# Optimization experiments

Measured on AMD Instinct MI355X. Metric: run time of the kernel, lower is better.

The kernel has to match this reference:

```python
import math
import jax, jax.numpy as jnp
import numpy as np

N_HEAD = 16
KNN = 4                     # config.knn_num
MEM_FRAC = 8.0              # config.mem_frac
INFLUENCE = 1.0             # config.knn_softmax_influence
RESID_FOUND = 0.5           # from set_resid_frac(resid_frac=0.5) (assumed split)
RESID_CURR = 0.5


def setup_inputs() -> dict:
    key = jax.random.key(0)
    ks = jax.random.split(key, 7)
    B, T, C, H, M = 1, 1024, 1024, N_HEAD, 8192
    d = C // H
    return {
        "x": jax.random.normal(ks[0], (B, T, C), jnp.float32),
        "c_attn_w": jax.random.normal(ks[1], (3 * C, C), jnp.float32) * 0.02,
        "c_attn_b": jax.random.normal(ks[2], (3 * C,), jnp.float32) * 0.01,
        "c_proj_w": jax.random.normal(ks[3], (C, C), jnp.float32) * 0.02,
        "c_proj_b": jax.random.normal(ks[4], (C,), jnp.float32) * 0.01,
        "key_store": jax.random.normal(ks[5], (H, M, d), jnp.float32),
        "value_store": jax.random.normal(ks[6], (H, M, d), jnp.float32),
    }


def _knn_get(att, k, q, v, key_store, value_store):
    # Faithful vectorized version of knn_get (batch must be 1, as in the
    # original whose scatter offsets i*t are only valid for b==1).
    B, H, T, d = k.shape
    scale = 1.0 / math.sqrt(d)
    # last-query attention row over all keys: (B,H,T)
    a = att[:, :, -1, :]
    # mem_frac thresholding (bookkeeping_frac falsy -> skipped)
    a = jnp.where(a < 1.0 / (MEM_FRAC * T), 0.0, a)
    sel = (a != 0.0)[0]                      # (H,T) selected positions
    kh, qh, vh = k[0], q[0], v[0]            # (H,T,d)
    # exact L2 search = faiss.IndexFlatL2: d2 = |k|^2 - 2 k.s + |s|^2
    d2 = (jnp.sum(kh * kh, -1, keepdims=True)
          - 2.0 * jnp.einsum('htd,hmd->htm', kh, key_store)
          + jnp.sum(key_store * key_store, -1)[:, None, :])   # (H,T,M)
    _, idx = jax.lax.top_k(-d2, KNN)         # (H,T,K) nearest neighbors
    idx = jnp.maximum(idx, 0)                # idx[idx<0]=0
    keys_f = jnp.take_along_axis(key_store[:, None, :, :], idx[..., None], axis=2)   # (H,T,K,d)
    vals_f = jnp.take_along_axis(value_store[:, None, :, :], idx[..., None], axis=2)
    # not resid_only: prepend current key/value -> stack size K+1
    keys_all = jnp.concatenate([kh[:, :, None, :], keys_f], axis=2)   # (H,T,S,d)
    vals_all = jnp.concatenate([vh[:, :, None, :], vals_f], axis=2)
    attf = jnp.einsum('htd,htsd->hts', qh, keys_all) * scale
    attf = jnp.where(jnp.isnan(attf), -jnp.inf, attf)
    w = jax.nn.softmax(attf * INFLUENCE, axis=-1)                     # softmax over the stack dim
    vals = jnp.einsum('hts,htsd->htd', w, vals_all)
    vals = vals * RESID_FOUND + vh * RESID_CURR                       # resid mix branch
    v_new = jnp.where(sel[..., None], vals, vh)                       # scatter back
    return v_new[None]                                                # (1,H,T,d)


def reference(x, c_attn_w, c_attn_b, c_proj_w, c_proj_b, key_store, value_store):
    B, T, C = x.shape
    H = key_store.shape[0]
    d = C // H
    qkv = x @ c_attn_w.T + c_attn_b
    q, k, v = jnp.split(qkv, 3, axis=2)
    heads = lambda t: t.reshape(B, T, H, d).transpose(0, 2, 1, 3)
    q, k, v = heads(q), heads(k), heads(v)
    logits = jnp.einsum('bhqd,bhkd->bhqk', q, k) * (1.0 / math.sqrt(d))
    causal = jnp.tril(jnp.ones((T, T), bool))
    logits = jnp.where(causal, logits, -jnp.inf)
    att = jax.nn.softmax(logits, axis=-1)
    # knn_get runs under torch.no_grad in the original
    v_new = jax.lax.stop_gradient(_knn_get(att, k, q, v, key_store, value_store))
    y = jnp.einsum('bhqk,bhkd->bhqd', att, v_new)   # dropout p=0 (eval)
    y = y.transpose(0, 2, 1, 3).reshape(B, T, C)
    return y @ c_proj_w.T + c_proj_b
```

## Files before the change

kernel.cpp:

```cpp
#include <hip/hip_runtime.h>
#include <math.h>

#define NH 16
#define TT 1024
#define CC 1024
#define DD 64
#define MM 8192
#define MQ 4
#define MQS (MM / MQ)

typedef __attribute__((ext_vector_type(8))) short short8;
typedef __attribute__((ext_vector_type(4))) float f32x4;

__device__ __forceinline__ float wredsum(float x) {
#pragma unroll
  for (int o = 32; o; o >>= 1) x += __shfl_xor(x, o);
  return x;
}
__device__ __forceinline__ unsigned int bf16rn(float x) {
  unsigned int u = __float_as_uint(x);
  return (u + 0x7fffu + ((u >> 16) & 1u)) >> 16;
}
__device__ __forceinline__ float bf16f(unsigned int h) {
  return __uint_as_float(h << 16);
}

__device__ __forceinline__ void ins4(float d, int i, float vd[4], int vi[4]) {
  if (d < vd[3] || (d == vd[3] && i < vi[3])) {
    vd[3] = d; vi[3] = i;
#pragma unroll
    for (int s = 3; s > 0; --s) {
      bool sw = (vd[s] < vd[s - 1]) || (vd[s] == vd[s - 1] && vi[s] < vi[s - 1]);
      if (sw) {
        float td = vd[s]; vd[s] = vd[s - 1]; vd[s - 1] = td;
        int ti = vi[s]; vi[s] = vi[s - 1]; vi[s - 1] = ti;
      }
    }
  }
}

__device__ __forceinline__ void stage_rows8_swz(const char* gRow0, size_t gStride, char* lds, int lane) {
  int rr = lane >> 3;
  int c = (lane & 7) ^ rr;
  __builtin_amdgcn_global_load_lds(
      (const __attribute__((address_space(1))) unsigned int*)(gRow0 + (size_t)rr * gStride + (c << 4)),
      (__attribute__((address_space(3))) unsigned int*)lds, 16, 0, 0);
}

__device__ __forceinline__ void conv_chunk(const float* __restrict__ src,
                                           char* __restrict__ hi, char* __restrict__ lo, int gc) {
  const float* p = src + ((size_t)gc << 3);
  float4 f0 = *(const float4*)p;
  float4 f1 = *(const float4*)(p + 4);
  float f[8] = {f0.x, f0.y, f0.z, f0.w, f1.x, f1.y, f1.z, f1.w};
  short8 hv, lv;
#pragma unroll
  for (int e = 0; e < 8; ++e) {
    unsigned hb = bf16rn(f[e]);
    hv[e] = (short)hb;
    lv[e] = (short)bf16rn(f[e] - bf16f(hb));
  }
  size_t off = (size_t)gc << 4;
  *(short8*)(hi + off) = hv;
  *(short8*)(lo + off) = lv;
}

__global__ void __launch_bounds__(256) convert_all(
    const float* __restrict__ x, char* __restrict__ xhi, char* __restrict__ xlo,
    const float* __restrict__ Wa, char* __restrict__ wahi, char* __restrict__ walo,
    const float* __restrict__ Wp, char* __restrict__ wphi, char* __restrict__ wplo)
{
  int b = blockIdx.x, tid = threadIdx.x;
  if (b < 512) conv_chunk(x, xhi, xlo, b * 256 + tid);
  else if (b < 2048) conv_chunk(Wa, wahi, walo, (b - 512) * 256 + tid);
  else conv_chunk(Wp, wphi, wplo, (b - 2048) * 256 + tid);
}

__global__ void __launch_bounds__(256) convert_kernel(
    const float* __restrict__ ks, char* __restrict__ khi,
    char* __restrict__ klo, float* __restrict__ kn2)
{
  int gc = blockIdx.x * 256 + threadIdx.x;
  const float* p = ks + ((size_t)gc << 3);
  float4 f0 = *(const float4*)p;
  float4 f1 = *(const float4*)(p + 4);
  float f[8] = {f0.x, f0.y, f0.z, f0.w, f1.x, f1.y, f1.z, f1.w};
  float s = 0.f;
  short8 hv, lv;
#pragma unroll
  for (int e = 0; e < 8; ++e) {
    s = fmaf(f[e], f[e], s);
    unsigned hb = bf16rn(f[e]);
    hv[e] = (short)hb;
    lv[e] = (short)bf16rn(f[e] - bf16f(hb));
  }
  size_t off = (size_t)gc << 4;
  *(short8*)(khi + off) = hv;
  *(short8*)(klo + off) = lv;
  s += __shfl_xor(s, 1);
  s += __shfl_xor(s, 2);
  s += __shfl_xor(s, 4);
  if ((threadIdx.x & 7) == 0) kn2[gc >> 3] = -0.5f * s;
}

__global__ void __launch_bounds__(256) gemm_hl(
    const char* __restrict__ Ahi, const char* __restrict__ Alo, int strideA, int aKb0, int aKbz,
    const char* __restrict__ Bhi, const char* __restrict__ Blo, int strideB, int bKb0, int bKbz,
    int kbBeg, int kbCnt, int kbzStep,
    float* __restrict__ Cf, long long czMul, int ldc,
    const float* __restrict__ bias, float scale)
{
  int bx = blockIdx.x, by = blockIdx.y, z = blockIdx.z;
  int n0 = bx * 128, m0 = by * 128;
  int tid = threadIdx.x, lane = tid & 63, w = tid >> 6;
  int wr = w >> 1, wc = w & 1;
  __shared__ __align__(16) char smem[65536];
  char* sAhi = smem;
  char* sAlo = smem + 16384;
  char* sBhi = smem + 32768;
  char* sBlo = smem + 49152;
  f32x4 acc[4][4];
#pragma unroll
  for (int i = 0; i < 4; ++i)
#pragma unroll
    for (int j = 0; j < 4; ++j) acc[i][j] = (f32x4){0.f, 0.f, 0.f, 0.f};

  int kb0 = kbBeg + z * kbzStep;
  int lr = lane & 15, lc = lane >> 4;
  for (int i = 0; i < kbCnt; ++i) {
    int kbA = aKb0 + z * aKbz + kb0 + i;
    int kbB = bKb0 + z * bKbz + kb0 + i;
    if (i) __syncthreads();
#pragma unroll
    for (int c8 = 0; c8 < 4; ++c8) {
      int r8 = w * 32 + c8 * 8;
      stage_rows8_swz(Ahi + (size_t)(m0 + r8) * strideA + (size_t)kbA * 128, strideA, sAhi + r8 * 128, lane);
      stage_rows8_swz(Alo + (size_t)(m0 + r8) * strideA + (size_t)kbA * 128, strideA, sAlo + r8 * 128, lane);
      stage_rows8_swz(Bhi + (size_t)(n0 + r8) * strideB + (size_t)kbB * 128, strideB, sBhi + r8 * 128, lane);
      stage_rows8_swz(Blo + (size_t)(n0 + r8) * strideB + (size_t)kbB * 128, strideB, sBlo + r8 * 128, lane);
    }
    __syncthreads();
#pragma unroll
    for (int kh = 0; kh < 2; ++kh) {
      short8 ah[4], al[4], bh[4], bl[4];
#pragma unroll
      for (int f = 0; f < 4; ++f) {
        int ra = wr * 64 + f * 16 + lr;
        int ca = ((kh * 4 + lc) ^ (ra & 7)) << 4;
        ah[f] = *(const short8*)(sAhi + ra * 128 + ca);
        al[f] = *(const short8*)(sAlo + ra * 128 + ca);
        int rb = wc * 64 + f * 16 + lr;
        int cb = ((kh * 4 + lc) ^ (rb & 7)) << 4;
        bh[f] = *(const short8*)(sBhi + rb * 128 + cb);
        bl[f] = *(const short8*)(sBlo + rb * 128 + cb);
      }
#pragma unroll
      for (int mi = 0; mi < 4; ++mi)
#pragma unroll
        for (int nj = 0; nj < 4; ++nj) {
          acc[mi][nj] = __builtin_amdgcn_mfma_f32_16x16x32_bf16(ah[mi], bh[nj], acc[mi][nj], 0, 0, 0);
          acc[mi][nj] = __builtin_amdgcn_mfma_f32_16x16x32_bf16(al[mi], bh[nj], acc[mi][nj], 0, 0, 0);
          acc[mi][nj] = __builtin_amdgcn_mfma_f32_16x16x32_bf16(ah[mi], bl[nj], acc[mi][nj], 0, 0, 0);
        }
    }
  }
#pragma unroll
  for (int mi = 0; mi < 4; ++mi)
#pragma unroll
    for (int nj = 0; nj < 4; ++nj)
#pragma unroll
      for (int r = 0; r < 4; ++r) {
        int m = m0 + wr * 64 + mi * 16 + lc * 4 + r;
        int n = n0 + wc * 64 + nj * 16 + lr;
        float v = acc[mi][nj][r] * scale;
        if (bias) v += bias[n];
        Cf[(size_t)z * czMul + (size_t)m * ldc + n] = v;
      }
}

__global__ void __launch_bounds__(256) reduce_qkv(
    const float* __restrict__ p, const float* __restrict__ bias,
    char* __restrict__ hi, char* __restrict__ lo)
{
  int gc = blockIdx.x * 256 + threadIdx.x;
  int t = gc / 384, c = gc - t * 384;
  const float* p0 = p + (size_t)t * 3072 + (c << 3);
  const float* p1 = p0 + (size_t)3072 * 1024;
  float4 a0 = *(const float4*)p0, a1 = *(const float4*)(p0 + 4);
  float4 b0 = *(const float4*)p1, b1 = *(const float4*)(p1 + 4);
  float4 bb0 = *(const float4*)(bias + (c << 3));
  float4 bb1 = *(const float4*)(bias + (c << 3) + 4);
  float f[8] = {a0.x + b0.x + bb0.x, a0.y + b0.y + bb0.y,
                a0.z + b0.z + bb0.z, a0.w + b0.w + bb0.w,
                a1.x + b1.x + bb1.x, a1.y + b1.y + bb1.y,
                a1.z + b1.z + bb1.z, a1.w + b1.w + bb1.w};
  short8 hv, lv;
#pragma unroll
  for (int e = 0; e < 8; ++e) {
    unsigned hb = bf16rn(f[e]);
    hv[e] = (short)hb;
    lv[e] = (short)bf16rn(f[e] - bf16f(hb));
  }
  size_t off = (size_t)gc << 4;
  *(short8*)(hi + off) = hv;
  *(short8*)(lo + off) = lv;
}

#define QSLDS 2304
__global__ void __launch_bounds__(512) qk_softmax(
    const char* __restrict__ qhi, const char* __restrict__ qlo,
    char* __restrict__ attB, float* __restrict__ attlast)
{
  int rb = blockIdx.x, h = blockIdx.y;
  int i0 = rb * 32;
  int tid = threadIdx.x, lane = tid & 63, w = tid >> 6;
  int wr = w >> 2, wcg = w & 3;
  int lr = lane & 15, lc = lane >> 4;
  __shared__ float redm[2][16][4];
  __shared__ float reds[2][16][4];
  __shared__ __align__(16) char tb[8][2 * QSLDS];

  int iq = i0 + wr * 16 + lr;
  short8 ah[2], al[2];
  {
    size_t qb = (size_t)iq * 6144 + h * 128;
#pragma unroll
    for (int kh = 0; kh < 2; ++kh) {
      size_t off = qb + ((kh * 4 + lc) << 4);
      ah[kh] = *(const short8*)(qhi + off);
      al[kh] = *(const short8*)(qlo + off);
    }
  }

  f32x4 acc[16];
#pragma unroll
  for (int nt = 0; nt < 16; ++nt) acc[nt] = (f32x4){0.f, 0.f, 0.f, 0.f};

  int maxj = i0 + 31;
#pragma unroll
  for (int nt = 0; nt < 16; ++nt) {
    if (wcg * 256 + nt * 16 <= maxj) {
      int jr = wcg * 256 + nt * 16 + lr;
      size_t kb = (size_t)jr * 6144 + 2048 + h * 128;
      short8 bh[2], bl[2];
#pragma unroll
      for (int kh = 0; kh < 2; ++kh) {
        size_t off = kb + ((kh * 4 + lc) << 4);
        bh[kh] = *(const short8*)(qhi + off);
        bl[kh] = *(const short8*)(qlo + off);
      }
#pragma unroll
      for (int kh = 0; kh < 2; ++kh) {
        acc[nt] = __builtin_amdgcn_mfma_f32_16x16x32_bf16(ah[kh], bh[kh], acc[nt], 0, 0, 0);
        acc[nt] = __builtin_amdgcn_mfma_f32_16x16x32_bf16(al[kh], bh[kh], acc[nt], 0, 0, 0);
        acc[nt] = __builtin_amdgcn_mfma_f32_16x16x32_bf16(ah[kh], bl[kh], acc[nt], 0, 0, 0);
      }
    }
  }

  int iv[4];
  float pmax[4];
#pragma unroll
  for (int r = 0; r < 4; ++r) {
    iv[r] = i0 + wr * 16 + lc * 4 + r;
    pmax[r] = -INFINITY;
  }
#pragma unroll
  for (int nt = 0; nt < 16; ++nt) {
    int j = wcg * 256 + nt * 16 + lr;
#pragma unroll
    for (int r = 0; r < 4; ++r) {
      float v = (j <= iv[r]) ? acc[nt][r] * 0.125f : -INFINITY;
      acc[nt][r] = v;
      pmax[r] = fmaxf(pmax[r], v);
    }
  }
#pragma unroll
  for (int o = 1; o <= 8; o <<= 1)
#pragma unroll
    for (int r = 0; r < 4; ++r) pmax[r] = fmaxf(pmax[r], __shfl_xor(pmax[r], o));
  if (lr == 0) {
#pragma unroll
    for (int r = 0; r < 4; ++r) redm[wr][lc * 4 + r][wcg] = pmax[r];
  }
  __syncthreads();
  float rowm[4];
#pragma unroll
  for (int r = 0; r < 4; ++r) {
    float* q = redm[wr][lc * 4 + r];
    rowm[r] = fmaxf(fmaxf(q[0], q[1]), fmaxf(q[2], q[3]));
  }

  float psum[4] = {0.f, 0.f, 0.f, 0.f};
#pragma unroll
  for (int nt = 0; nt < 16; ++nt)
#pragma unroll
    for (int r = 0; r < 4; ++r) {
      float e = __expf(acc[nt][r] - rowm[r]);
      acc[nt][r] = e;
      psum[r] += e;
    }
#pragma unroll
  for (int o = 1; o <= 8; o <<= 1)
#pragma unroll
    for (int r = 0; r < 4; ++r) psum[r] += __shfl_xor(psum[r], o);
  if (lr == 0) {
#pragma unroll
    for (int r = 0; r < 4; ++r) reds[wr][lc * 4 + r][wcg] = psum[r];
  }
  __syncthreads();
  float inv[4];
#pragma unroll
  for (int r = 0; r < 4; ++r) {
    float* q = reds[wr][lc * 4 + r];
    inv[r] = 1.0f / (q[0] + q[1] + q[2] + q[3]);
  }

  char* mybuf = tb[w];
  int iv0 = i0 + wr * 16;
#pragma unroll
  for (int cc = 0; cc < 4; ++cc) {
#pragma unroll
    for (int q = 0; q < 4; ++q) {
      int nt = cc * 4 + q;
      int col = q * 16 + lr;
#pragma unroll
      for (int r = 0; r < 4; ++r) {
        int row = lc * 4 + r;
        float v = acc[nt][r] * inv[r];
        unsigned hb = bf16rn(v);
        unsigned lb = bf16rn(v - bf16f(hb));
        *(unsigned short*)(mybuf + row * 144 + col * 2) = (unsigned short)hb;
        *(unsigned short*)(mybuf + QSLDS + row * 144 + col * 2) = (unsigned short)lb;
        if (iv[r] == 1023) attlast[(h << 10) + wcg * 256 + cc * 64 + col] = v;
      }
    }
    __syncthreads();
#pragma unroll
    for (int half = 0; half < 2; ++half) {
      int rr = (lane >> 3) + half * 8;
      int c = lane & 7;
      int rowg = iv0 + rr;
      uint4 hv = *(const uint4*)(mybuf + rr * 144 + c * 16);
      uint4 lv = *(const uint4*)(mybuf + QSLDS + rr * 144 + c * 16);
      size_t basep = ((size_t)h << 22) + ((size_t)rowg << 12)
                   + (size_t)(((wcg << 2) + cc) << 7) + (size_t)(c << 4);
      *(uint4*)(attB + basep) = hv;
      *(uint4*)(attB + basep + 2048) = lv;
    }
    __syncthreads();
  }
}

#define BUFB 16384

#define TOPK_STEP(PAR, DO_STAGE)                                              \
  {                                                                           \
    if (DO_STAGE) {                                                           \
      _Pragma("unroll")                                                       \
      for (int i2 = 0; i2 < 4; ++i2) {                                        \
        __builtin_amdgcn_global_load_lds(                                     \
            (const __attribute__((address_space(1))) unsigned int*)stsrc[i2], \
            (__attribute__((address_space(3))) unsigned int*)(stdst[i2] + ((PAR) ^ 16384)), \
            16, 0, 0);                                                        \
        stsrc[i2] += 8192;                                                    \
      }                                                                       \
    }                                                                         \
    f32x4 acc[4];                                                             \
    _Pragma("unroll")                                                         \
    for (int ms = 0; ms < 4; ++ms)                                            \
      acc[ms] = *(const f32x4*)(knp + ms * 64);                               \
    knp += 256;                                                               \
    _Pragma("unroll")                                                         \
    for (int ms = 0; ms < 4; ++ms) {                                          \
      short8 ah0 = *(const short8*)(frg[ms * 2 + 0] + (PAR));                 \
      short8 al0 = *(const short8*)(frg[ms * 2 + 0] + (PAR) + 8192);          \
      short8 ah1 = *(const short8*)(frg[ms * 2 + 1] + (PAR));                 \
      short8 al1 = *(const short8*)(frg[ms * 2 + 1] + (PAR) + 8192);          \
      acc[ms] = __builtin_amdgcn_mfma_f32_16x16x32_bf16(ah0, bhi[0], acc[ms], 0, 0, 0); \
      acc[ms] = __builtin_amdgcn_mfma_f32_16x16x32_bf16(al0, bhi[0], acc[ms], 0, 0, 0); \
      acc[ms] = __builtin_amdgcn_mfma_f32_16x16x32_bf16(ah0, blo[0], acc[ms], 0, 0, 0); \
      acc[ms] = __builtin_amdgcn_mfma_f32_16x16x32_bf16(ah1, bhi[1], acc[ms], 0, 0, 0); \
      acc[ms] = __builtin_amdgcn_mfma_f32_16x16x32_bf16(al1, bhi[1], acc[ms], 0, 0, 0); \
      acc[ms] = __builtin_amdgcn_mfma_f32_16x16x32_bf16(ah1, blo[1], acc[ms], 0, 0, 0); \
    }                                                                         \
    float pk[16];                                                             \
    _Pragma("unroll")                                                         \
    for (int ms = 0; ms < 4; ++ms)                                            \
      _Pragma("unroll")                                                       \
      for (int r = 0; r < 4; ++r) {                                           \
        unsigned u = __float_as_uint(acc[ms][r]);                             \
        pk[ms * 4 + r] = __uint_as_float((u & ~15u) | (unsigned)(ms * 4 + r)); \
      }                                                                       \
    float mx = pk[0];                                                         \
    _Pragma("unroll")                                                         \
    for (int c = 1; c < 16; ++c) mx = fmaxf(mx, pk[c]);                       \
    while (mx > ba[3]) {                                                      \
      unsigned pb = __float_as_uint(mx);                                      \
      int cl = pb & 15;                                                       \
      ba[3] = mx; bi_[3] = mg0 + ((cl & 12) << 2) + (cl & 3);                 \
      _Pragma("unroll")                                                       \
      for (int s = 3; s > 0; --s)                                             \
        if (ba[s] > ba[s - 1]) {                                              \
          float td = ba[s]; ba[s] = ba[s - 1]; ba[s - 1] = td;                \
          int ti = bi_[s]; bi_[s] = bi_[s - 1]; bi_[s - 1] = ti;              \
        }                                                                     \
      _Pragma("unroll")                                                       \
      for (int c2 = 0; c2 < 16; ++c2)                                         \
        if (pk[c2] == mx) pk[c2] = -3.0e38f;                                  \
      mx = pk[0];                                                             \
      _Pragma("unroll")                                                       \
      for (int c2 = 1; c2 < 16; ++c2) mx = fmaxf(mx, pk[c2]);                 \
    }                                                                         \
    mg0 += 64;                                                                \
    __syncthreads();                                                          \
  }

__global__ void __launch_bounds__(256, 4) topk_mfma(
    const char* __restrict__ qhi, const char* __restrict__ qlo,
    const char* __restrict__ khi, const char* __restrict__ klo,
    const float* __restrict__ kn2, float* __restrict__ pd, int* __restrict__ pi)
{
  int bid = blockIdx.x;
  int h = bid & 15, ttile = (bid >> 4) & 15, mq = bid >> 8;
  int tid = threadIdx.x, lane = tid & 63, w = tid >> 6;
  int t0 = ttile * 64 + w * 16;
  __shared__ __align__(16) char smem[2 * BUFB];

  short8 bhi[2], blo[2];
  {
    int t = t0 + (lane & 15);
    size_t rb = (size_t)t * 6144 + 2048 + h * 128;
#pragma unroll
    for (int kh = 0; kh < 2; ++kh) {
      size_t off = rb + ((kh * 4 + (lane >> 4)) << 4);
      bhi[kh] = *(const short8*)(qhi + off);
      blo[kh] = *(const short8*)(qlo + off);
    }
  }

  const char* ghi = khi + ((size_t)h * MM + (size_t)mq * MQS) * 128;
  const char* glo = klo + ((size_t)h * MM + (size_t)mq * MQS) * 128;
  const char* knp = (const char*)(kn2 + (size_t)h * MM + (size_t)mq * MQS + ((lane >> 4) << 2));

  float ba[4] = {-3.0e38f, -3.0e38f, -3.0e38f, -3.0e38f};
  int   bi_[4] = {-1, -1, -1, -1};

  const char* stsrc[4];
  char* stdst[4];
  {
    int rr = lane >> 3;
    size_t laneoff = (size_t)rr * 128 + (((lane & 7) ^ rr) << 4);
#pragma unroll
    for (int i2 = 0; i2 < 4; ++i2) {
      int s = w * 4 + i2;
      stsrc[i2] = ((s < 8) ? (ghi + s * 1024) : (glo + (s - 8) * 1024)) + laneoff;
      stdst[i2] = smem + s * 1024;
    }
  }
  char* frg[8];
#pragma unroll
  for (int ms = 0; ms < 4; ++ms)
#pragma unroll
    for (int kh = 0; kh < 2; ++kh) {
      int mloc = ms * 16 + (lane & 15);
      int c = kh * 4 + (lane >> 4);
      frg[ms * 2 + kh] = smem + mloc * 128 + ((c ^ (mloc & 7)) << 4);
    }

#pragma unroll
  for (int i2 = 0; i2 < 4; ++i2) {
    __builtin_amdgcn_global_load_lds(
        (const __attribute__((address_space(1))) unsigned int*)stsrc[i2],
        (__attribute__((address_space(3))) unsigned int*)stdst[i2], 16, 0, 0);
    stsrc[i2] += 8192;
  }
  __syncthreads();

  int mg0 = mq * MQS + ((lane >> 4) << 2);
  for (int it2 = 0; it2 < 16; ++it2) {
    TOPK_STEP(0, true)
    TOPK_STEP(16384, (it2 < 15))
  }

  float bd[4];
#pragma unroll
  for (int s = 0; s < 4; ++s) bd[s] = ba[s] * -2.0f;
#pragma unroll
  for (int st = 16; st <= 32; st <<= 1) {
    float sd[4]; int si[4];
#pragma unroll
    for (int s = 0; s < 4; ++s) {
      sd[s] = __shfl_xor(bd[s], st);
      si[s] = __shfl_xor(bi_[s], st);
    }
#pragma unroll
    for (int s = 0; s < 4; ++s) ins4(sd[s], si[s], bd, bi_);
  }
  if (lane < 16) {
    size_t o = (((size_t)mq * NH + h) * TT + (t0 + lane)) * 4;
#pragma unroll
    for (int s = 0; s < 4; ++s) { pd[o + s] = bd[s]; pi[o + s] = bi_[s]; }
  }
}

__global__ void __launch_bounds__(1024) knn_attend(
    const char* __restrict__ qhi, const char* __restrict__ qlo,
    const float* __restrict__ attlast,
    const float* __restrict__ pd, const int* __restrict__ pi,
    const float* __restrict__ kstore, const float* __restrict__ vstore,
    char* __restrict__ vThi, char* __restrict__ vTlo)
{
  __shared__ __align__(16) unsigned short hiT[64][72];
  __shared__ __align__(16) unsigned short loT[64][72];
  int tid = threadIdx.x, lane = tid & 63, w = tid >> 6;
  int h = blockIdx.x >> 4, t0 = (blockIdx.x & 15) << 6;

#pragma unroll
  for (int i = 0; i < 4; ++i) {
    int t = t0 + w * 4 + i;
    int g = (h << 10) + t;

    float fd[4]; int fi[4];
    {
      size_t o = ((size_t)(lane & 3) * (NH * TT) + g) * 4;
#pragma unroll
      for (int s = 0; s < 4; ++s) { fd[s] = pd[o + s]; fi[s] = pi[o + s]; }
#pragma unroll
      for (int st = 1; st <= 2; st <<= 1) {
        float sd[4]; int si[4];
#pragma unroll
        for (int s = 0; s < 4; ++s) {
          sd[s] = __shfl_xor(fd[s], st);
          si[s] = __shfl_xor(fi[s], st);
        }
#pragma unroll
        for (int s = 0; s < 4; ++s) ins4(sd[s], si[s], fd, fi);
      }
    }

    size_t rb = (size_t)t * 6144 + h * 128 + lane * 2;
    float q = bf16f(*(const unsigned short*)(qhi + rb)) + bf16f(*(const unsigned short*)(qlo + rb));
    float k = bf16f(*(const unsigned short*)(qhi + rb + 2048)) + bf16f(*(const unsigned short*)(qlo + rb + 2048));
    float v = bf16f(*(const unsigned short*)(qhi + rb + 4096)) + bf16f(*(const unsigned short*)(qlo + rb + 4096));
    float al = attlast[g];
    bool sel = al >= (1.0f / 8192.0f);

    float attf[5], vf[5];
    attf[0] = wredsum(q * k) * 0.125f;
    vf[0] = v;
#pragma unroll
    for (int s = 1; s < 5; ++s) {
      int m = fi[s - 1];
      const float* kp = kstore + ((size_t)h * MM + m) * DD;
      const float* vp = vstore + ((size_t)h * MM + m) * DD;
      attf[s] = wredsum(q * kp[lane]) * 0.125f;
      vf[s] = vp[lane];
    }
    float mx = attf[0];
#pragma unroll
    for (int s = 1; s < 5; ++s) mx = fmaxf(mx, attf[s]);
    float wgt[5], sum = 0.f;
#pragma unroll
    for (int s = 0; s < 5; ++s) { wgt[s] = __expf(attf[s] - mx); sum += wgt[s]; }
    float inv = 1.0f / sum;
    float vals = 0.f;
#pragma unroll
    for (int s = 0; s < 5; ++s) vals = fmaf(wgt[s] * inv, vf[s], vals);
    float r = 0.5f * vals + 0.5f * v;
    float vn = sel ? r : v;

    unsigned hb = bf16rn(vn);
    hiT[lane][t - t0] = (unsigned short)hb;
    loT[lane][t - t0] = (unsigned short)bf16rn(vn - bf16f(hb));
  }
  __syncthreads();

  int half = tid >> 9;
  int idx = tid & 511;
  int r = idx >> 3, c = idx & 7;
  const unsigned short* src = half ? &loT[r][c * 8] : &hiT[r][c * 8];
  uint4 vv = *(const uint4*)src;
  char* dst = (half ? vTlo : vThi) + (size_t)((h << 6) + r) * 2048 + ((size_t)t0 << 1) + (c << 4);
  *(uint4*)dst = vv;
}

__global__ void __launch_bounds__(256) gemm_attv(
    const char* __restrict__ attB, const char* __restrict__ vThi, const char* __restrict__ vTlo,
    char* __restrict__ Yhi, char* __restrict__ Ylo)
{
  int h = blockIdx.y, m0 = blockIdx.x * 128;
  const char* aBase = attB + (size_t)h * 4194304;
  int tid = threadIdx.x, lane = tid & 63, w = tid >> 6;
  int wr = w >> 1, wc = w & 1;
  __shared__ __align__(16) char smem[49152];
  char* sAhi = smem;
  char* sAlo = smem + 16384;
  char* sBhi = smem + 32768;
  char* sBlo = smem + 40960;
  f32x4 acc[4][2];
#pragma unroll
  for (int i = 0; i < 4; ++i)
#pragma unroll
    for (int j = 0; j < 2; ++j) acc[i][j] = (f32x4){0.f, 0.f, 0.f, 0.f};
  int lr = lane & 15, lc = lane >> 4;
  int kbEnd = ((m0 + 127) >> 6) + 1;
  if (kbEnd > 16) kbEnd = 16;
  for (int kb = 0; kb < kbEnd; ++kb) {
    if (kb) __syncthreads();
#pragma unroll
    for (int c8 = 0; c8 < 4; ++c8) {
      int r8 = w * 32 + c8 * 8;
      stage_rows8_swz(aBase + (size_t)(m0 + r8) * 4096 + (size_t)kb * 128, 4096, sAhi + r8 * 128, lane);
      stage_rows8_swz(aBase + (size_t)(m0 + r8) * 4096 + 2048 + (size_t)kb * 128, 4096, sAlo + r8 * 128, lane);
    }
#pragma unroll
    for (int c8 = 0; c8 < 2; ++c8) {
      int r8 = w * 16 + c8 * 8;
      stage_rows8_swz(vThi + (size_t)((h << 6) + r8) * 2048 + (size_t)kb * 128, 2048, sBhi + r8 * 128, lane);
      stage_rows8_swz(vTlo + (size_t)((h << 6) + r8) * 2048 + (size_t)kb * 128, 2048, sBlo + r8 * 128, lane);
    }
    __syncthreads();
#pragma unroll
    for (int kh = 0; kh < 2; ++kh) {
      short8 ah[4], al[4], bh[2], bl[2];
#pragma unroll
      for (int f = 0; f < 4; ++f) {
        int ra = wr * 64 + f * 16 + lr;
        int ca = ((kh * 4 + lc) ^ (ra & 7)) << 4;
        ah[f] = *(const short8*)(sAhi + ra * 128 + ca);
        al[f] = *(const short8*)(sAlo + ra * 128 + ca);
      }
#pragma unroll
      for (int f = 0; f < 2; ++f) {
        int rbr = wc * 32 + f * 16 + lr;
        int cb = ((kh * 4 + lc) ^ (rbr & 7)) << 4;
        bh[f] = *(const short8*)(sBhi + rbr * 128 + cb);
        bl[f] = *(const short8*)(sBlo + rbr * 128 + cb);
      }
#pragma unroll
      for (int mi = 0; mi < 4; ++mi)
#pragma unroll
        for (int nj = 0; nj < 2; ++nj) {
          acc[mi][nj] = __builtin_amdgcn_mfma_f32_16x16x32_bf16(ah[mi], bh[nj], acc[mi][nj], 0, 0, 0);
          acc[mi][nj] = __builtin_amdgcn_mfma_f32_16x16x32_bf16(al[mi], bh[nj], acc[mi][nj], 0, 0, 0);
          acc[mi][nj] = __builtin_amdgcn_mfma_f32_16x16x32_bf16(ah[mi], bl[nj], acc[mi][nj], 0, 0, 0);
        }
    }
  }
#pragma unroll
  for (int mi = 0; mi < 4; ++mi)
#pragma unroll
    for (int nj = 0; nj < 2; ++nj)
#pragma unroll
      for (int r = 0; r < 4; ++r) {
        int m = m0 + wr * 64 + mi * 16 + lc * 4 + r;
        int n = (h << 6) + wc * 32 + nj * 16 + lr;
        float v = acc[mi][nj][r];
        unsigned hb = bf16rn(v);
        size_t off = ((size_t)m * 1024 + n) * 2;
        *(unsigned short*)(Yhi + off) = (unsigned short)hb;
        *(unsigned short*)(Ylo + off) = (unsigned short)bf16rn(v - bf16f(hb));
      }
}

__global__ void __launch_bounds__(256) reduce_bias(
    const float* __restrict__ p, const float* __restrict__ bias, float* __restrict__ out)
{
  int i4 = blockIdx.x * 256 + threadIdx.x;
  const float4* P = (const float4*)p;
  float4 a = P[i4], b = P[i4 + 262144], c = P[i4 + 524288], d = P[i4 + 786432];
  float4 bb = ((const float4*)bias)[i4 & 255];
  float4 o;
  o.x = a.x + b.x + c.x + d.x + bb.x;
  o.y = a.y + b.y + c.y + d.y + bb.y;
  o.z = a.z + b.z + c.z + d.z + bb.z;
  o.w = a.w + b.w + c.w + d.w + bb.w;
  ((float4*)out)[i4] = o;
}

extern "C" void kernel_launch(void* const* d_in, const int* in_sizes, int n_in,
                              void* d_out, int out_size, void* d_ws, size_t ws_size,
                              hipStream_t stream) {
  (void)in_sizes; (void)n_in; (void)out_size; (void)ws_size;
  const float* x  = (const float*)d_in[0];
  const float* Wa = (const float*)d_in[1];
  const float* ba = (const float*)d_in[2];
  const float* Wp = (const float*)d_in[3];
  const float* bp = (const float*)d_in[4];
  const float* Ks = (const float*)d_in[5];
  const float* Vs = (const float*)d_in[6];
  float* out = (float*)d_out;

  char* base = (char*)d_ws;
  char* xhi  = base;
  char* xlo  = base + 0x200000;
  char* wahi = base + 0x400000;
  char* walo = base + 0xA00000;
  char* khi  = base + 0x1000000;
  char* klo  = base + 0x2000000;
  float* qkvp = (float*)(base + 0x1000000);
  char*  attB = base;
  float* pout = (float*)base;
  char* tail = base + 0x4000000;
  char* qhi = tail;
  char* qlo = tail + 0x600000;
  float* attlast = (float*)(tail + 0xC00000);
  float* kn2     = (float*)(tail + 0xC10000);
  float* pd      = (float*)(tail + 0xC90000);
  int*   pi      = (int*)(tail + 0xE90000);
  char* vThi = tail + 0x1090000;
  char* vTlo = tail + 0x1290000;
  char* yhi  = tail + 0x1490000;
  char* ylo  = tail + 0x1690000;
  char* wphi = tail + 0x1890000;
  char* wplo = tail + 0x1A90000;

  hipLaunchKernelGGL(convert_all, dim3(2560), dim3(256), 0, stream,
                     x, xhi, xlo, Wa, wahi, walo, Wp, wphi, wplo);
  hipLaunchKernelGGL(gemm_hl, dim3(24, 8, 2), dim3(256), 0, stream,
                     (const char*)xhi, (const char*)xlo, 2048, 0, 0,
                     (const char*)wahi, (const char*)walo, 2048, 0, 0,
                     0, 8, 8,
                     qkvp, 3145728LL, 3072,
                     (const float*)nullptr, 1.0f);
  hipLaunchKernelGGL(reduce_qkv, dim3(1536), dim3(256), 0, stream, qkvp, ba, qhi, qlo);
  hipLaunchKernelGGL(convert_kernel, dim3(NH * MM * 8 / 256), dim3(256), 0, stream, Ks, khi, klo, kn2);
  hipLaunchKernelGGL(topk_mfma, dim3(16 * 16 * MQ), dim3(256), 0, stream,
                     (const char*)qhi, (const char*)qlo, (const char*)khi, (const char*)klo,
                     kn2, pd, pi);
  hipLaunchKernelGGL(qk_softmax, dim3(32, 16), dim3(512), 0, stream,
                     (const char*)qhi, (const char*)qlo, attB, attlast);
  hipLaunchKernelGGL(knn_attend, dim3(256), dim3(1024), 0, stream,
                     (const char*)qhi, (const char*)qlo, attlast, pd, pi, Ks, Vs, vThi, vTlo);
  hipLaunchKernelGGL(gemm_attv, dim3(8, 16), dim3(256), 0, stream,
                     (const char*)attB, (const char*)vThi, (const char*)vTlo, yhi, ylo);
  hipLaunchKernelGGL(gemm_hl, dim3(8, 8, 4), dim3(256), 0, stream,
                     (const char*)yhi, (const char*)ylo, 2048, 0, 0,
                     (const char*)wphi, (const char*)wplo, 2048, 0, 0,
                     0, 4, 4,
                     pout, 1048576LL, 1024,
                     (const float*)nullptr, 1.0f);
  hipLaunchKernelGGL(reduce_bias, dim3(1024), dim3(256), 0, stream, pout, bp, out);
}
```

Baseline: 225.9 us.

## Replace split-K GEMMs and reduce kernels with fused-epilogue GEMMs, merge convert kernels

Drops the split-K QKV and output projection GEMMs and their separate reduce kernels. In their place come dedicated GEMMs with smaller tiles: 64x128 for QKV, with bias add and hi/lo bf16 split done in the epilogue through LDS, and 64x64 for the output projection, with bias written straight to the output. The key-store conversion is also folded into the convert_all launch. The aim is to cut launches and the float partial-sum round trips through global memory. The cost is less parallelism per tile and the full K loop running in each block.

```diff
diff --git a/kernel.cpp b/kernel.cpp
--- a/kernel.cpp
+++ b/kernel.cpp
@@ -68,19 +68,15 @@
 __global__ void __launch_bounds__(256) convert_all(
     const float* __restrict__ x, char* __restrict__ xhi, char* __restrict__ xlo,
     const float* __restrict__ Wa, char* __restrict__ wahi, char* __restrict__ walo,
-    const float* __restrict__ Wp, char* __restrict__ wphi, char* __restrict__ wplo)
+    const float* __restrict__ Wp, char* __restrict__ wphi, char* __restrict__ wplo,
+    const float* __restrict__ ks, char* __restrict__ khi, char* __restrict__ klo,
+    float* __restrict__ kn2)
 {
   int b = blockIdx.x, tid = threadIdx.x;
-  if (b < 512) conv_chunk(x, xhi, xlo, b * 256 + tid);
-  else if (b < 2048) conv_chunk(Wa, wahi, walo, (b - 512) * 256 + tid);
-  else conv_chunk(Wp, wphi, wplo, (b - 2048) * 256 + tid);
-}
-
-__global__ void __launch_bounds__(256) convert_kernel(
-    const float* __restrict__ ks, char* __restrict__ khi,
-    char* __restrict__ klo, float* __restrict__ kn2)
-{
-  int gc = blockIdx.x * 256 + threadIdx.x;
+  if (b < 512) { conv_chunk(x, xhi, xlo, b * 256 + tid); return; }
+  if (b < 2048) { conv_chunk(Wa, wahi, walo, (b - 512) * 256 + tid); return; }
+  if (b < 2560) { conv_chunk(Wp, wphi, wplo, (b - 2048) * 256 + tid); return; }
+  int gc = (b - 2560) * 256 + tid;
   const float* p = ks + ((size_t)gc << 3);
   float4 f0 = *(const float4*)p;
   float4 f1 = *(const float4*)(p + 4);
@@ -100,62 +96,63 @@
   s += __shfl_xor(s, 1);
   s += __shfl_xor(s, 2);
   s += __shfl_xor(s, 4);
-  if ((threadIdx.x & 7) == 0) kn2[gc >> 3] = -0.5f * s;
-}
-
-__global__ void __launch_bounds__(256) gemm_hl(
-    const char* __restrict__ Ahi, const char* __restrict__ Alo, int strideA, int aKb0, int aKbz,
-    const char* __restrict__ Bhi, const char* __restrict__ Blo, int strideB, int bKb0, int bKbz,
-    int kbBeg, int kbCnt, int kbzStep,
-    float* __restrict__ Cf, long long czMul, int ldc,
-    const float* __restrict__ bias, float scale)
+  if ((tid & 7) == 0) kn2[gc >> 3] = -0.5f * s;
+}
+
+__global__ void __launch_bounds__(256) gemm_qkv(
+    const char* __restrict__ xhi, const char* __restrict__ xlo,
+    const char* __restrict__ wahi, const char* __restrict__ walo,
+    const float* __restrict__ ba, char* __restrict__ qhi, char* __restrict__ qlo)
 {
-  int bx = blockIdx.x, by = blockIdx.y, z = blockIdx.z;
-  int n0 = bx * 128, m0 = by * 128;
+  int n0 = blockIdx.x * 128, m0 = blockIdx.y * 64;
   int tid = threadIdx.x, lane = tid & 63, w = tid >> 6;
   int wr = w >> 1, wc = w & 1;
-  __shared__ __align__(16) char smem[65536];
+  int lr = lane & 15, lc = lane >> 4;
+  __shared__ __align__(16) char smem[49152];
   char* sAhi = smem;
-  char* sAlo = smem + 16384;
-  char* sBhi = smem + 32768;
-  char* sBlo = smem + 49152;
-  f32x4 acc[4][4];
-#pragma unroll
-  for (int i = 0; i < 4; ++i)
+  char* sAlo = smem + 8192;
+  char* sBhi = smem + 16384;
+  char* sBlo = smem + 32768;
+  f32x4 acc[2][4];
+#pragma unroll
+  for (int i = 0; i < 2; ++i)
 #pragma unroll
     for (int j = 0; j < 4; ++j) acc[i][j] = (f32x4){0.f, 0.f, 0.f, 0.f};
 
-  int kb0 = kbBeg + z * kbzStep;
-  int lr = lane & 15, lc = lane >> 4;
-  for (int i = 0; i < kbCnt; ++i) {
-    int kbA = aKb0 + z * aKbz + kb0 + i;
-    int kbB = bKb0 + z * bKbz + kb0 + i;
-    if (i) __syncthreads();
+  for (int kb = 0; kb < 16; ++kb) {
+    if (kb) __syncthreads();
+#pragma unroll
+    for (int c8 = 0; c8 < 2; ++c8) {
+      int r8 = w * 16 + c8 * 8;
+      stage_rows8_swz(xhi + (size_t)(m0 + r8) * 2048 + (size_t)kb * 128, 2048, sAhi + r8 * 128, lane);
+      stage_rows8_swz(xlo + (size_t)(m0 + r8) * 2048 + (size_t)kb * 128, 2048, sAlo + r8 * 128, lane);
+    }
 #pragma unroll
     for (int c8 = 0; c8 < 4; ++c8) {
       int r8 = w * 32 + c8 * 8;
-      stage_rows8_swz(Ahi + (size_t)(m0 + r8) * strideA + (size_t)kbA * 128, strideA, sAhi + r8 * 128, lane);
-      stage_rows8_swz(Alo + (size_t)(m0 + r8) * strideA + (size_t)kbA * 128, strideA, sAlo + r8 * 128, lane);
-      stage_rows8_swz(Bhi + (size_t)(n0 + r8) * strideB + (size_t)kbB * 128, strideB, sBhi + r8 * 128, lane);
-      stage_rows8_swz(Blo + (size_t)(n0 + r8) * strideB + (size_t)kbB * 128, strideB, sBlo + r8 * 128, lane);
+      stage_rows8_swz(wahi + (size_t)(n0 + r8) * 2048 + (size_t)kb * 128, 2048, sBhi + r8 * 128, lane);
+      stage_rows8_swz(walo + (size_t)(n0 + r8) * 2048 + (size_t)kb * 128, 2048, sBlo + r8 * 128, lane);
     }
     __syncthreads();
 #pragma unroll
     for (int kh = 0; kh < 2; ++kh) {
-      short8 ah[4], al[4], bh[4], bl[4];
-#pragma unroll
-      for (int f = 0; f < 4; ++f) {
-        int ra = wr * 64 + f * 16 + lr;
+      short8 ah[2], al[2], bh[4], bl[4];
+#pragma unroll
+      for (int mi = 0; mi < 2; ++mi) {
+        int ra = wr * 32 + mi * 16 + lr;
         int ca = ((kh * 4 + lc) ^ (ra & 7)) << 4;
-        ah[f] = *(const short8*)(sAhi + ra * 128 + ca);
-        al[f] = *(const short8*)(sAlo + ra * 128 + ca);
-        int rb = wc * 64 + f * 16 + lr;
+        ah[mi] = *(const short8*)(sAhi + ra * 128 + ca);
+        al[mi] = *(const short8*)(sAlo + ra * 128 + ca);
+      }
+#pragma unroll
+      for (int nj = 0; nj < 4; ++nj) {
+        int rb = wc * 64 + nj * 16 + lr;
         int cb = ((kh * 4 + lc) ^ (rb & 7)) << 4;
-        bh[f] = *(const short8*)(sBhi + rb * 128 + cb);
-        bl[f] = *(const short8*)(sBlo + rb * 128 + cb);
-      }
-#pragma unroll
-      for (int mi = 0; mi < 4; ++mi)
+        bh[nj] = *(const short8*)(sBhi + rb * 128 + cb);
+        bl[nj] = *(const short8*)(sBlo + rb * 128 + cb);
+      }
+#pragma unroll
+      for (int mi = 0; mi < 2; ++mi)
 #pragma unroll
         for (int nj = 0; nj < 4; ++nj) {
           acc[mi][nj] = __builtin_amdgcn_mfma_f32_16x16x32_bf16(ah[mi], bh[nj], acc[mi][nj], 0, 0, 0);
@@ -164,46 +161,31 @@
         }
     }
   }
-#pragma unroll
-  for (int mi = 0; mi < 4; ++mi)
+
+  __syncthreads();
+  char* hbuf = smem + w * 9216;
+  char* lbuf = hbuf + 4608;
+#pragma unroll
+  for (int mi = 0; mi < 2; ++mi)
 #pragma unroll
     for (int nj = 0; nj < 4; ++nj)
 #pragma unroll
       for (int r = 0; r < 4; ++r) {
-        int m = m0 + wr * 64 + mi * 16 + lc * 4 + r;
-        int n = n0 + wc * 64 + nj * 16 + lr;
-        float v = acc[mi][nj][r] * scale;
-        if (bias) v += bias[n];
-        Cf[(size_t)z * czMul + (size_t)m * ldc + n] = v;
-      }
-}
-
-__global__ void __launch_bounds__(256) reduce_qkv(
-    const float* __restrict__ p, const float* __restrict__ bias,
-    char* __restrict__ hi, char* __restrict__ lo)
-{
-  int gc = blockIdx.x * 256 + threadIdx.x;
-  int t = gc / 384, c = gc - t * 384;
-  const float* p0 = p + (size_t)t * 3072 + (c << 3);
-  const float* p1 = p0 + (size_t)3072 * 1024;
-  float4 a0 = *(const float4*)p0, a1 = *(const float4*)(p0 + 4);
-  float4 b0 = *(const float4*)p1, b1 = *(const float4*)(p1 + 4);
-  float4 bb0 = *(const float4*)(bias + (c << 3));
-  float4 bb1 = *(const float4*)(bias + (c << 3) + 4);
-  float f[8] = {a0.x + b0.x + bb0.x, a0.y + b0.y + bb0.y,
-                a0.z + b0.z + bb0.z, a0.w + b0.w + bb0.w,
-                a1.x + b1.x + bb1.x, a1.y + b1.y + bb1.y,
-                a1.z + b1.z + bb1.z, a1.w + b1.w + bb1.w};
-  short8 hv, lv;
-#pragma unroll
-  for (int e = 0; e < 8; ++e) {
-    unsigned hb = bf16rn(f[e]);
-    hv[e] = (short)hb;
-    lv[e] = (short)bf16rn(f[e] - bf16f(hb));
-  }
-  size_t off = (size_t)gc << 4;
-  *(short8*)(hi + off) = hv;
-  *(short8*)(lo + off) = lv;
+        int row = mi * 16 + lc * 4 + r;
+        int col = nj * 16 + lr;
+        float v = acc[mi][nj][r] + ba[n0 + wc * 64 + col];
+        unsigned hb = bf16rn(v);
+        *(unsigned short*)(hbuf + row * 144 + col * 2) = (unsigned short)hb;
+        *(unsigned short*)(lbuf + row * 144 + col * 2) = (unsigned short)bf16rn(v - bf16f(hb));
+      }
+#pragma unroll
+  for (int ps = 0; ps < 4; ++ps) {
+    int rr = ps * 8 + (lane >> 3);
+    int c = lane & 7;
+    size_t gb = ((size_t)(m0 + wr * 32 + rr) * 3072 + n0 + wc * 64) * 2 + (c << 4);
+    *(uint4*)(qhi + gb) = *(const uint4*)(hbuf + rr * 144 + c * 16);
+    *(uint4*)(qlo + gb) = *(const uint4*)(lbuf + rr * 144 + c * 16);
+  }
 }
 
 #define QSLDS 2304
@@ -664,19 +646,74 @@
       }
 }
 
-__global__ void __launch_bounds__(256) reduce_bias(
-    const float* __restrict__ p, const float* __restrict__ bias, float* __restrict__ out)
+__global__ void __launch_bounds__(256) gemm_out(
+    const char* __restrict__ yhi, const char* __restrict__ ylo,
+    const char* __restrict__ wphi, const char* __restrict__ wplo,
+    const float* __restrict__ bp, float* __restrict__ out)
 {
-  int i4 = blockIdx.x * 256 + threadIdx.x;
-  const float4* P = (const float4*)p;
-  float4 a = P[i4], b = P[i4 + 262144], c = P[i4 + 524288], d = P[i4 + 786432];
-  float4 bb = ((const float4*)bias)[i4 & 255];
-  float4 o;
-  o.x = a.x + b.x + c.x + d.x + bb.x;
-  o.y = a.y + b.y + c.y + d.y + bb.y;
-  o.z = a.z + b.z + c.z + d.z + bb.z;
-  o.w = a.w + b.w + c.w + d.w + bb.w;
-  ((float4*)out)[i4] = o;
+  int n0 = blockIdx.x * 64, m0 = blockIdx.y * 64;
+  int tid = threadIdx.x, lane = tid & 63, w = tid >> 6;
+  int wr = w >> 1, wc = w & 1;
+  int lr = lane & 15, lc = lane >> 4;
+  __shared__ __align__(16) char smem[32768];
+  char* sAhi = smem;
+  char* sAlo = smem + 8192;
+  char* sBhi = smem + 16384;
+  char* sBlo = smem + 24576;
+  f32x4 acc[2][2];
+#pragma unroll
+  for (int i = 0; i < 2; ++i)
+#pragma unroll
+    for (int j = 0; j < 2; ++j) acc[i][j] = (f32x4){0.f, 0.f, 0.f, 0.f};
+
+  for (int kb = 0; kb < 16; ++kb) {
+    if (kb) __syncthreads();
+#pragma unroll
+    for (int c8 = 0; c8 < 2; ++c8) {
+      int r8 = w * 16 + c8 * 8;
+      stage_rows8_swz(yhi + (size_t)(m0 + r8) * 2048 + (size_t)kb * 128, 2048, sAhi + r8 * 128, lane);
+      stage_rows8_swz(ylo + (size_t)(m0 + r8) * 2048 + (size_t)kb * 128, 2048, sAlo + r8 * 128, lane);
+      stage_rows8_swz(wphi + (size_t)(n0 + r8) * 2048 + (size_t)kb * 128, 2048, sBhi + r8 * 128, lane);
+      stage_rows8_swz(wplo + (size_t)(n0 + r8) * 2048 + (size_t)kb * 128, 2048, sBlo + r8 * 128, lane);
+    }
+    __syncthreads();
+#pragma unroll
+    for (int kh = 0; kh < 2; ++kh) {
+      short8 ah[2], al[2], bh[2], bl[2];
+#pragma unroll
+      for (int mi = 0; mi < 2; ++mi) {
+        int ra = wr * 32 + mi * 16 + lr;
+        int ca = ((kh * 4 + lc) ^ (ra & 7)) << 4;
+        ah[mi] = *(const short8*)(sAhi + ra * 128 + ca);
+        al[mi] = *(const short8*)(sAlo + ra * 128 + ca);
+      }
+#pragma unroll
+      for (int nj = 0; nj < 2; ++nj) {
+        int rb = wc * 32 + nj * 16 + lr;
+        int cb = ((kh * 4 + lc) ^ (rb & 7)) << 4;
+        bh[nj] = *(const short8*)(sBhi + rb * 128 + cb);
+        bl[nj] = *(const short8*)(sBlo + rb * 128 + cb);
+      }
+#pragma unroll
+      for (int mi = 0; mi < 2; ++mi)
+#pragma unroll
+        for (int nj = 0; nj < 2; ++nj) {
+          acc[mi][nj] = __builtin_amdgcn_mfma_f32_16x16x32_bf16(ah[mi], bh[nj], acc[mi][nj], 0, 0, 0);
+          acc[mi][nj] = __builtin_amdgcn_mfma_f32_16x16x32_bf16(al[mi], bh[nj], acc[mi][nj], 0, 0, 0);
+          acc[mi][nj] = __builtin_amdgcn_mfma_f32_16x16x32_bf16(ah[mi], bl[nj], acc[mi][nj], 0, 0, 0);
+        }
+    }
+  }
+#pragma unroll
+  for (int mi = 0; mi < 2; ++mi)
+#pragma unroll
+    for (int nj = 0; nj < 2; ++nj)
+#pragma unroll
+      for (int r = 0; r < 4; ++r) {
+        int m = m0 + wr * 32 + mi * 16 + lc * 4 + r;
+        int n = n0 + wc * 32 + nj * 16 + lr;
+        out[(size_t)m * 1024 + n] = acc[mi][nj][r] + bp[n];
+      }
 }
 
 extern "C" void kernel_launch(void* const* d_in, const int* in_sizes, int n_in,
@@ -699,9 +736,7 @@
   char* walo = base + 0xA00000;
   char* khi  = base + 0x1000000;
   char* klo  = base + 0x2000000;
-  float* qkvp = (float*)(base + 0x1000000);
   char*  attB = base;
-  float* pout = (float*)base;
   char* tail = base + 0x4000000;
   char* qhi = tail;
   char* qlo = tail + 0x600000;
@@ -716,16 +751,11 @@
   char* wphi = tail + 0x1890000;
   char* wplo = tail + 0x1A90000;
 
-  hipLaunchKernelGGL(convert_all, dim3(2560), dim3(256), 0, stream,
-                     x, xhi, xlo, Wa, wahi, walo, Wp, wphi, wplo);
-  hipLaunchKernelGGL(gemm_hl, dim3(24, 8, 2), dim3(256), 0, stream,
-                     (const char*)xhi, (const char*)xlo, 2048, 0, 0,
-                     (const char*)wahi, (const char*)walo, 2048, 0, 0,
-                     0, 8, 8,
-                     qkvp, 3145728LL, 3072,
-                     (const float*)nullptr, 1.0f);
-  hipLaunchKernelGGL(reduce_qkv, dim3(1536), dim3(256), 0, stream, qkvp, ba, qhi, qlo);
-  hipLaunchKernelGGL(convert_kernel, dim3(NH * MM * 8 / 256), dim3(256), 0, stream, Ks, khi, klo, kn2);
+  hipLaunchKernelGGL(convert_all, dim3(6656), dim3(256), 0, stream,
+                     x, xhi, xlo, Wa, wahi, walo, Wp, wphi, wplo, Ks, khi, klo, kn2);
+  hipLaunchKernelGGL(gemm_qkv, dim3(24, 16), dim3(256), 0, stream,
+                     (const char*)xhi, (const char*)xlo, (const char*)wahi, (const char*)walo,
+                     ba, qhi, qlo);
   hipLaunchKernelGGL(topk_mfma, dim3(16 * 16 * MQ), dim3(256), 0, stream,
                      (const char*)qhi, (const char*)qlo, (const char*)khi, (const char*)klo,
                      kn2, pd, pi);
@@ -735,11 +765,7 @@
                      (const char*)qhi, (const char*)qlo, attlast, pd, pi, Ks, Vs, vThi, vTlo);
   hipLaunchKernelGGL(gemm_attv, dim3(8, 16), dim3(256), 0, stream,
                      (const char*)attB, (const char*)vThi, (const char*)vTlo, yhi, ylo);
-  hipLaunchKernelGGL(gemm_hl, dim3(8, 8, 4), dim3(256), 0, stream,
-                     (const char*)yhi, (const char*)ylo, 2048, 0, 0,
-                     (const char*)wphi, (const char*)wplo, 2048, 0, 0,
-                     0, 4, 4,
-                     pout, 1048576LL, 1024,
-                     (const float*)nullptr, 1.0f);
-  hipLaunchKernelGGL(reduce_bias, dim3(1024), dim3(256), 0, stream, pout, bp, out);
-}
+  hipLaunchKernelGGL(gemm_out, dim3(16, 16), dim3(256), 0, stream,
+                     (const char*)yhi, (const char*)ylo, (const char*)wphi, (const char*)wplo,
+                     bp, out);
+}
```

Result: faster. 217.0 us (-3.9%).
